# Kernel tuning notes

Hardware: AMD Instinct MI355X
Metric: run time of the kernel (lower is better)

Reference implementation:

```python
import jax, jax.numpy as jnp
import numpy as np


def setup_inputs() -> dict:
    key = jax.random.key(0)
    k1, k2 = jax.random.split(key)
    x = jax.random.normal(k1, (32, 64, 64, 64), dtype=jnp.float32)
    codebook = jax.random.normal(k2, (1024, 64), dtype=jnp.float32)
    return {"x": x, "codebook": codebook}


def reference(x, codebook):
    # x: (B, D, H, W)  codebook: (K, D)
    B, D = x.shape[0], x.shape[1]
    spatial = x.shape[2:]
    flat = x.reshape(B, D, -1).transpose(0, 2, 1)  # (B, N, D)
    dot = jnp.einsum("bnd,kd->bnk", flat, codebook)
    cb_norm = jnp.sum(codebook * codebook, axis=-1)  # (K,)
    indices = jnp.argmin(cb_norm[None, None, :] - 2.0 * dot, axis=-1)  # (B, N)
    quantized = codebook[indices]  # (B, N, D) gather
    out = quantized.transpose(0, 2, 1).reshape(x.shape)
    return out, indices.reshape((B,) + spatial)
```

## Files before the change

### kernel.cpp

```cpp
#include <hip/hip_runtime.h>


typedef _Float16 f16x8 __attribute__((ext_vector_type(8)));
typedef float    f32x4 __attribute__((ext_vector_type(4)));

#define VQ_D    64
#define VQ_HW   4096
#define VQ_NPOS 131072
#define SC      2048.0f
#define EPS_Q   24
#define CHB     16640
#define CHBP    17664
#define WS_CBN  66560
#define WS_CBT  67584
#define WS_CNT  133120
#define WS_LIST 133124

__global__ __launch_bounds__(256)
void vq_prep(const float* __restrict__ cb, float* __restrict__ ws)
{
    const int tid = threadIdx.x;
    const int blk = blockIdx.x;
    if (blk < 64) {
        const int it   = blk * 256 + tid;
        const int ct   = it >> 8;
        const int s    = (it >> 6) & 3;
        const int lane = it & 63;
        const int ks   = s & 1, isR = s >> 1;
        const int n    = ct * 16 + (lane & 15);
        const int k0   = ks * 32 + (lane >> 4) * 8;
        const float* src = cb + n * 64 + k0;
        f16x8 o;
        #pragma unroll
        for (int j = 0; j < 8; ++j) {
            const float b = src[j];
            const _Float16 bh = (_Float16)b;
            o[j] = isR ? (_Float16)((b - (float)bh) * (-2.0f * SC))
                       : (_Float16)(-2.0f * (float)bh);
        }
        *(f16x8*)((char*)ws + (size_t)(ct >> 2) * CHB + (ct & 3) * 4096
                            + s * 1024 + lane * 16) = o;
    } else if (blk < 128) {
        const int it = (blk - 64) * 256 + tid;
        const int k = it >> 4, j4 = it & 15;
        ((float4*)(ws + WS_CBT))[j4 * 1024 + k] = ((const float4*)cb)[it];
    } else {
        const int k = (blk - 128) * 256 + tid;
        const float4* row = (const float4*)(cb + k * 64);
        float a0 = 0.f, a1 = 0.f, a2 = 0.f, a3 = 0.f;
        #pragma unroll
        for (int j = 0; j < 16; ++j) {
            const float4 c = row[j];
            a0 = fmaf(c.x, c.x, a0); a1 = fmaf(c.y, c.y, a1);
            a2 = fmaf(c.z, c.z, a2); a3 = fmaf(c.w, c.w, a3);
        }
        const float cn = (a0 + a1) + (a2 + a3);
        ws[WS_CBN + k] = cn;
        const int ct = k >> 4, i = k & 15;
        *(float*)((char*)ws + (size_t)(ct >> 2) * CHB + 16384
                            + (ct & 3) * 64 + i * 4) = cn * 2048.0f;
        if (k == 0) ((int*)ws)[WS_CNT] = 0;
    }
}

#define GLOAD_LDS(GP, LP)                                                     \
    __builtin_amdgcn_global_load_lds(                                         \
        (const __attribute__((address_space(1))) unsigned int*)(GP),          \
        (__attribute__((address_space(3))) unsigned int*)(LP), 16, 0, 0)

#define STAGE(GS, BOFF)                                                       \
    {                                                                         \
        char* ld_ = (char*)bbuf + (BOFF) + wv * 1024;                         \
        const char* gs_ = (GS) + wv * 1024;                                   \
        GLOAD_LDS(gs_,         ld_);                                          \
        GLOAD_LDS(gs_ + 4096,  ld_ + 4096);                                   \
        GLOAD_LDS(gs_ + 8192,  ld_ + 8192);                                   \
        GLOAD_LDS(gs_ + 12288, ld_ + 12288);                                  \
        if (wv == 0 && lane < 16)                                             \
            GLOAD_LDS((GS) + 16384, (char*)bbuf + (BOFF) + 16384);            \
    }

#define CT_BODY(BOFF, SLOT, CTG)                                              \
    {                                                                         \
        const f16x8 B0 = *(const f16x8*)(lp + (BOFF) + (SLOT) * 4096);        \
        const f16x8 B1 = *(const f16x8*)(lp + (BOFF) + (SLOT) * 4096 + 1024); \
        const f16x8 R0 = *(const f16x8*)(lp + (BOFF) + (SLOT) * 4096 + 2048); \
        const f16x8 R1 = *(const f16x8*)(lp + (BOFF) + (SLOT) * 4096 + 3072); \
        const float cvq = *(const float*)(cp + (BOFF) + (SLOT) * 64);         \
        const f32x4 Ci = {cvq, cvq, cvq, cvq};                                \
        f32x4 pa0 = __builtin_amdgcn_mfma_f32_16x16x32_f16(Ak[0][0], B0, Ci,    0,0,0); \
        f32x4 pb0 = __builtin_amdgcn_mfma_f32_16x16x32_f16(Ak[0][1], B1, zero4, 0,0,0); \
        f32x4 pa1 = __builtin_amdgcn_mfma_f32_16x16x32_f16(Ak[1][0], B0, Ci,    0,0,0); \
        f32x4 pb1 = __builtin_amdgcn_mfma_f32_16x16x32_f16(Ak[1][1], B1, zero4, 0,0,0); \
        pa0 = __builtin_amdgcn_mfma_f32_16x16x32_f16(Ah[0][0], R0, pa0, 0,0,0); \
        pb0 = __builtin_amdgcn_mfma_f32_16x16x32_f16(Ah[0][1], R1, pb0, 0,0,0); \
        pa1 = __builtin_amdgcn_mfma_f32_16x16x32_f16(Ah[1][0], R0, pa1, 0,0,0); \
        pb1 = __builtin_amdgcn_mfma_f32_16x16x32_f16(Ah[1][1], R1, pb1, 0,0,0); \
        pa0 = __builtin_amdgcn_mfma_f32_16x16x32_f16(Ra[0][0], B0, pa0, 0,0,0); \
        pb0 = __builtin_amdgcn_mfma_f32_16x16x32_f16(Ra[0][1], B1, pb0, 0,0,0); \
        pa1 = __builtin_amdgcn_mfma_f32_16x16x32_f16(Ra[1][0], B0, pa1, 0,0,0); \
        pb1 = __builtin_amdgcn_mfma_f32_16x16x32_f16(Ra[1][1], B1, pb1, 0,0,0); \
        const int cbase_ = (CTG) * 16 + m;                                    \
        _Pragma("unroll")                                                     \
        for (int r = 0; r < 4; ++r) {                                         \
            const float q0_ = pa0[r] + pb0[r];                                \
            const int k0_ = ((int)q0_ << 10) | cbase_;                        \
            int m0_;                                                          \
            asm("v_med3_i32 %0, %1, %2, %3"                                   \
                : "=v"(m0_) : "v"(k0_), "v"(d1[0][r]), "v"(d2[0][r]));        \
            d2[0][r] = m0_;                                                   \
            d1[0][r] = (k0_ < d1[0][r]) ? k0_ : d1[0][r];                     \
            const float q1_ = pa1[r] + pb1[r];                                \
            const int k1_ = ((int)q1_ << 10) | cbase_;                        \
            int m1_;                                                          \
            asm("v_med3_i32 %0, %1, %2, %3"                                   \
                : "=v"(m1_) : "v"(k1_), "v"(d1[1][r]), "v"(d2[1][r]));        \
            d2[1][r] = m1_;                                                   \
            d1[1][r] = (k1_ < d1[1][r]) ? k1_ : d1[1][r];                     \
        }                                                                     \
        __builtin_amdgcn_sched_barrier(0x100);    \
    }

__global__ __launch_bounds__(256, 4)
void vq_main(const float* __restrict__ x,
             const float* __restrict__ cb,
             float* __restrict__ ws,
             float* __restrict__ out,
             float* __restrict__ idx_out)
{
    __shared__ f16x8 bbuf[2 * (CHBP / 16)];
    __shared__ int   sk[128];
    __shared__ int   smg[128];

    const int tid  = threadIdx.x;
    const int lane = tid & 63;
    const int wv   = tid >> 6;
    const int m    = lane & 15;
    const int q    = lane >> 4;

    const int p0 = blockIdx.x * 128;
    const int b  = p0 >> 12;
    const int n0 = p0 & (VQ_HW - 1);
    const float* xw = x + (size_t)b * (VQ_D * VQ_HW) + n0 + wv * 32;

    const char* gs = (const char*)ws + lane * 16;

    STAGE(gs, 0)

    f16x8 Ah[2][2], Ak[2][2], Ra[2][2];
    #pragma unroll
    for (int tl = 0; tl < 2; ++tl)
        #pragma unroll
        for (int ks = 0; ks < 2; ++ks) {
            f16x8 h8, k8, r8;
            #pragma unroll
            for (int j = 0; j < 8; ++j) {
                const float v = xw[(size_t)(ks * 32 + q * 8 + j) * VQ_HW + tl * 16 + m];
                const _Float16 vh = (_Float16)v;
                h8[j] = vh;
                k8[j] = (_Float16)((float)vh * 2048.0f);
                r8[j] = (_Float16)((v - (float)vh) * SC);
            }
            Ah[tl][ks] = h8; Ak[tl][ks] = k8; Ra[tl][ks] = r8;
        }

    int d1[2][4], d2[2][4];
    #pragma unroll
    for (int tl = 0; tl < 2; ++tl)
        #pragma unroll
        for (int r = 0; r < 4; ++r) { d1[tl][r] = 0x7FFFFFFF; d2[tl][r] = 0x7FFFFFFF; }

    const f32x4 zero4 = {0.f, 0.f, 0.f, 0.f};
    const char* lp = (const char*)bbuf + lane * 16;
    const char* cp = (const char*)bbuf + 16384 + m * 4;

    for (int it8 = 0; it8 < 8; ++it8) {
        const int cg = it8 * 8;
        __syncthreads();
        STAGE(gs + CHB, CHBP)
        CT_BODY(0, 0, cg + 0)
        CT_BODY(0, 1, cg + 1)
        CT_BODY(0, 2, cg + 2)
        CT_BODY(0, 3, cg + 3)
        __syncthreads();
        if (it8 < 7) STAGE(gs + 2 * CHB, 0)
        CT_BODY(CHBP, 0, cg + 4)
        CT_BODY(CHBP, 1, cg + 5)
        CT_BODY(CHBP, 2, cg + 6)
        CT_BODY(CHBP, 3, cg + 7)
        gs += 2 * CHB;
    }

    #pragma unroll
    for (int off = 1; off < 16; off <<= 1)
        #pragma unroll
        for (int tl = 0; tl < 2; ++tl)
            #pragma unroll
            for (int r = 0; r < 4; ++r) {
                const int od1 = __shfl_xor(d1[tl][r], off, 64);
                const int od2 = __shfl_xor(d2[tl][r], off, 64);
                const int mx  = (d1[tl][r] > od1) ? d1[tl][r] : od1;
                const int mn2 = (d2[tl][r] < od2) ? d2[tl][r] : od2;
                d2[tl][r] = (mx < mn2) ? mx : mn2;
                d1[tl][r] = (d1[tl][r] < od1) ? d1[tl][r] : od1;
            }

    if (m == 0) {
        #pragma unroll
        for (int tl = 0; tl < 2; ++tl)
            #pragma unroll
            for (int r = 0; r < 4; ++r) {
                const int li = wv * 32 + tl * 16 + q * 4 + r;
                sk[li]  = d1[tl][r] & 1023;
                smg[li] = (d2[tl][r] >> 10) - (d1[tl][r] >> 10);
            }
    }
    __syncthreads();

    const int pos  = tid & 127;
    const int half = tid >> 7;
    const int bk   = sk[pos];
    if (half == 0) {
        idx_out[p0 + pos] = (float)bk;
        if (smg[pos] < EPS_Q) {
            const int slot = atomicAdd((int*)ws + WS_CNT, 1);
            ((int*)ws)[WS_LIST + slot] = p0 + pos;
        }
    }
    const float4* cr = (const float4*)(cb + (size_t)bk * VQ_D) + half * 8;
    float* ob = out + (size_t)b * (VQ_D * VQ_HW) + (size_t)(half * 32) * VQ_HW + n0 + pos;
    #pragma unroll
    for (int d4 = 0; d4 < 8; ++d4) {
        const float4 v = cr[d4];
        ob[(size_t)(d4 * 4 + 0) * VQ_HW] = v.x;
        ob[(size_t)(d4 * 4 + 1) * VQ_HW] = v.y;
        ob[(size_t)(d4 * 4 + 2) * VQ_HW] = v.z;
        ob[(size_t)(d4 * 4 + 3) * VQ_HW] = v.w;
    }
}

__global__ __launch_bounds__(64)
void vq_rescan(const float* __restrict__ x,
               const float* __restrict__ cb,
               const float* __restrict__ ws,
               float* __restrict__ out,
               float* __restrict__ idx_out)
{
    __shared__ float xs[VQ_D];
    const int lane = threadIdx.x;
    const int cnt  = ((const int*)ws)[WS_CNT];
    const int* list = (const int*)ws + WS_LIST;
    const float*  cnb  = ws + WS_CBN;
    const float4* cbT4 = (const float4*)(ws + WS_CBT);

    for (int i = blockIdx.x; i < cnt; i += gridDim.x) {
        const int p = list[i];
        const int b = p >> 12, n = p & (VQ_HW - 1);
        xs[lane] = x[(size_t)b * (VQ_D * VQ_HW) + (size_t)lane * VQ_HW + n];
        __syncthreads();
        float4 xr[16];
        #pragma unroll
        for (int j = 0; j < 16; ++j) xr[j] = ((const float4*)xs)[j];

        float bd = 3.4e38f; int bk = 0;
        #pragma unroll 4
        for (int t = 0; t < 16; ++t) {
            const int code = t * 64 + lane;
            float a0 = 0.f, a1 = 0.f, a2 = 0.f, a3 = 0.f;
            #pragma unroll
            for (int j4 = 0; j4 < 16; ++j4) {
                const float4 c = cbT4[j4 * 1024 + code];
                a0 = fmaf(xr[j4].x, c.x, a0); a1 = fmaf(xr[j4].y, c.y, a1);
                a2 = fmaf(xr[j4].z, c.z, a2); a3 = fmaf(xr[j4].w, c.w, a3);
            }
            const float dist = fmaf(-2.0f, (a0 + a1) + (a2 + a3), cnb[code]);
            if (dist < bd) { bd = dist; bk = code; }
        }
        #pragma unroll
        for (int off = 1; off < 64; off <<= 1) {
            const float od = __shfl_xor(bd, off, 64);
            const int   ok = __shfl_xor(bk, off, 64);
            if (od < bd || (od == bd && ok < bk)) { bd = od; bk = ok; }
        }
        out[(size_t)b * (VQ_D * VQ_HW) + (size_t)lane * VQ_HW + n] = cb[(size_t)bk * VQ_D + lane];
        if (lane == 0) idx_out[p] = (float)bk;
        __syncthreads();
    }
}

extern "C" void kernel_launch(void* const* d_in, const int* in_sizes, int n_in,
                              void* d_out, int out_size, void* d_ws, size_t ws_size,
                              hipStream_t stream) {
    const float* x  = (const float*)d_in[0];
    const float* cb = (const float*)d_in[1];
    float* out = (float*)d_out;
    float* idx = out + (size_t)VQ_NPOS * VQ_D;
    float* ws  = (float*)d_ws;

    vq_prep  <<<dim3(132),  dim3(256), 0, stream>>>(cb, ws);
    vq_main  <<<dim3(1024), dim3(256), 0, stream>>>(x, cb, ws, out, idx);
    vq_rescan<<<dim3(1024), dim3(64),  0, stream>>>(x, cb, ws, out, idx);
}
```

Measured before the change: 160.2 us.

## Restructure codebook staging into 4-deep LDS ring with fine-grained vmcnt waits

Replaces the double-buffered 4-tile chunk staging with a 4-slot ring buffer of 2-tile (8 KB) chunks, prefetching three chunks ahead and using explicit s_waitcnt vmcnt plus s_barrier instead of full __syncthreads. The scaled codebook norms are loaded once into a dedicated LDS array, which simplifies the workspace layout to plain linear order. MFMA sections are wrapped in s_setprio to favor matrix issue. This aims to hide global-to-LDS latency better and cut barrier stalls, at the cost of more barriers per codebook tile, a fully unrolled 32-step loop, and reliance on hand-counted vmcnt values being correct.

```diff
diff --git a/kernel.cpp b/kernel.cpp
--- a/kernel.cpp
+++ b/kernel.cpp
@@ -9,9 +9,8 @@
 #define VQ_NPOS 131072
 #define SC      2048.0f
 #define EPS_Q   24
-#define CHB     16640
-#define CHBP    17664
-#define WS_CBN  66560
+#define WS_CBN  65536
+#define WS_CNQ  66560
 #define WS_CBT  67584
 #define WS_CNT  133120
 #define WS_LIST 133124
@@ -38,8 +37,7 @@
             o[j] = isR ? (_Float16)((b - (float)bh) * (-2.0f * SC))
                        : (_Float16)(-2.0f * (float)bh);
         }
-        *(f16x8*)((char*)ws + (size_t)(ct >> 2) * CHB + (ct & 3) * 4096
-                            + s * 1024 + lane * 16) = o;
+        ((f16x8*)ws)[it] = o;
     } else if (blk < 128) {
         const int it = (blk - 64) * 256 + tid;
         const int k = it >> 4, j4 = it & 15;
@@ -56,9 +54,7 @@
         }
         const float cn = (a0 + a1) + (a2 + a3);
         ws[WS_CBN + k] = cn;
-        const int ct = k >> 4, i = k & 15;
-        *(float*)((char*)ws + (size_t)(ct >> 2) * CHB + 16384
-                            + (ct & 3) * 64 + i * 4) = cn * 2048.0f;
+        ws[WS_CNQ + k] = cn * 2048.0f;
         if (k == 0) ((int*)ws)[WS_CNT] = 0;
     }
 }
@@ -68,26 +64,24 @@
         (const __attribute__((address_space(1))) unsigned int*)(GP),          \
         (__attribute__((address_space(3))) unsigned int*)(LP), 16, 0, 0)
 
-#define STAGE(GS, BOFF)                                                       \
+#define STAGE2(CK, BOFF)                                                      \
     {                                                                         \
-        char* ld_ = (char*)bbuf + (BOFF) + wv * 1024;                         \
-        const char* gs_ = (GS) + wv * 1024;                                   \
-        GLOAD_LDS(gs_,         ld_);                                          \
-        GLOAD_LDS(gs_ + 4096,  ld_ + 4096);                                   \
-        GLOAD_LDS(gs_ + 8192,  ld_ + 8192);                                   \
-        GLOAD_LDS(gs_ + 12288, ld_ + 12288);                                  \
-        if (wv == 0 && lane < 16)                                             \
-            GLOAD_LDS((GS) + 16384, (char*)bbuf + (BOFF) + 16384);            \
-    }
-
-#define CT_BODY(BOFF, SLOT, CTG)                                              \
+        const char* gs_ = (const char*)ws + (size_t)(CK) * 8192               \
+                          + wv * 2048 + lane * 16;                            \
+        char* ld_ = (char*)bbuf + (BOFF) + wv * 2048;                         \
+        GLOAD_LDS(gs_, ld_);                                                  \
+        GLOAD_LDS(gs_ + 1024, ld_ + 1024);                                    \
+    }
+
+#define CT_BODY(BOFF, CI, CTG)                                                \
     {                                                                         \
-        const f16x8 B0 = *(const f16x8*)(lp + (BOFF) + (SLOT) * 4096);        \
-        const f16x8 B1 = *(const f16x8*)(lp + (BOFF) + (SLOT) * 4096 + 1024); \
-        const f16x8 R0 = *(const f16x8*)(lp + (BOFF) + (SLOT) * 4096 + 2048); \
-        const f16x8 R1 = *(const f16x8*)(lp + (BOFF) + (SLOT) * 4096 + 3072); \
-        const float cvq = *(const float*)(cp + (BOFF) + (SLOT) * 64);         \
+        const f16x8 B0 = *(const f16x8*)(lp + (BOFF) + (CI) * 4096);          \
+        const f16x8 B1 = *(const f16x8*)(lp + (BOFF) + (CI) * 4096 + 1024);   \
+        const f16x8 R0 = *(const f16x8*)(lp + (BOFF) + (CI) * 4096 + 2048);   \
+        const f16x8 R1 = *(const f16x8*)(lp + (BOFF) + (CI) * 4096 + 3072);   \
+        const float cvq = cnq_lds[(CTG) * 16 + m];                            \
         const f32x4 Ci = {cvq, cvq, cvq, cvq};                                \
+        __builtin_amdgcn_s_setprio(1);                                        \
         f32x4 pa0 = __builtin_amdgcn_mfma_f32_16x16x32_f16(Ak[0][0], B0, Ci,    0,0,0); \
         f32x4 pb0 = __builtin_amdgcn_mfma_f32_16x16x32_f16(Ak[0][1], B1, zero4, 0,0,0); \
         f32x4 pa1 = __builtin_amdgcn_mfma_f32_16x16x32_f16(Ak[1][0], B0, Ci,    0,0,0); \
@@ -100,6 +94,7 @@
         pb0 = __builtin_amdgcn_mfma_f32_16x16x32_f16(Ra[0][1], B1, pb0, 0,0,0); \
         pa1 = __builtin_amdgcn_mfma_f32_16x16x32_f16(Ra[1][0], B0, pa1, 0,0,0); \
         pb1 = __builtin_amdgcn_mfma_f32_16x16x32_f16(Ra[1][1], B1, pb1, 0,0,0); \
+        __builtin_amdgcn_s_setprio(0);                                        \
         const int cbase_ = (CTG) * 16 + m;                                    \
         _Pragma("unroll")                                                     \
         for (int r = 0; r < 4; ++r) {                                         \
@@ -121,6 +116,16 @@
         __builtin_amdgcn_sched_barrier(0x100);    \
     }
 
+#define ITER_T(VMSTR, DOSTAGE, T)                                             \
+    {                                                                         \
+        asm volatile("s_waitcnt " VMSTR ::: "memory");                        \
+        __builtin_amdgcn_s_barrier();                                         \
+        if (DOSTAGE) STAGE2((T) + 3, (((T) + 3) & 3) * 8192)                  \
+        const int base_ = ((T) & 3) * 8192;                                   \
+        CT_BODY(base_, 0, (T) * 2)                                            \
+        CT_BODY(base_, 1, (T) * 2 + 1)                                        \
+    }
+
 __global__ __launch_bounds__(256, 4)
 void vq_main(const float* __restrict__ x,
              const float* __restrict__ cb,
@@ -128,7 +133,8 @@
              float* __restrict__ out,
              float* __restrict__ idx_out)
 {
-    __shared__ f16x8 bbuf[2 * (CHBP / 16)];
+    __shared__ f16x8 bbuf[4 * 512];
+    __shared__ float cnq_lds[1024];
     __shared__ int   sk[128];
     __shared__ int   smg[128];
 
@@ -143,9 +149,11 @@
     const int n0 = p0 & (VQ_HW - 1);
     const float* xw = x + (size_t)b * (VQ_D * VQ_HW) + n0 + wv * 32;
 
-    const char* gs = (const char*)ws + lane * 16;
-
-    STAGE(gs, 0)
+    STAGE2(0, 0)
+    STAGE2(1, 8192)
+    STAGE2(2, 16384)
+
+    ((float4*)cnq_lds)[tid] = ((const float4*)(ws + WS_CNQ))[tid];
 
     f16x8 Ah[2][2], Ak[2][2], Ra[2][2];
     #pragma unroll
@@ -172,24 +180,14 @@
 
     const f32x4 zero4 = {0.f, 0.f, 0.f, 0.f};
     const char* lp = (const char*)bbuf + lane * 16;
-    const char* cp = (const char*)bbuf + 16384 + m * 4;
-
-    for (int it8 = 0; it8 < 8; ++it8) {
-        const int cg = it8 * 8;
-        __syncthreads();
-        STAGE(gs + CHB, CHBP)
-        CT_BODY(0, 0, cg + 0)
-        CT_BODY(0, 1, cg + 1)
-        CT_BODY(0, 2, cg + 2)
-        CT_BODY(0, 3, cg + 3)
-        __syncthreads();
-        if (it8 < 7) STAGE(gs + 2 * CHB, 0)
-        CT_BODY(CHBP, 0, cg + 4)
-        CT_BODY(CHBP, 1, cg + 5)
-        CT_BODY(CHBP, 2, cg + 6)
-        CT_BODY(CHBP, 3, cg + 7)
-        gs += 2 * CHB;
-    }
+
+    __syncthreads();
+
+    for (int t = 0; t < 29; ++t)
+        ITER_T("vmcnt(4)", 1, t)
+    ITER_T("vmcnt(4)", 0, 29)
+    ITER_T("vmcnt(2)", 0, 30)
+    ITER_T("vmcnt(0)", 0, 31)
 
     #pragma unroll
     for (int off = 1; off < 16; off <<= 1)
```

Result: no change. 158.5 us (-1.0%).
